# Optimization experiments

Hardware: AMD Instinct MI355X
Metric: run time of the kernel (lower is better)

Reference implementation:

```python
import jax, jax.numpy as jnp
import numpy as np

H, W = 576, 640            # image_height, image_width
V = 5                      # visible_patch_width (z-buffer visibility window)
P = 7                      # color_path_width (color splat window)
EPS = 1e-5                 # epsilon in splat weight denominator
BIG = 1e10                 # empty-pixel depth sentinel


def setup_inputs():
    key = jax.random.key(0)
    ks = jax.random.split(key, 6)
    B, N = 1, 200000
    x = jax.random.uniform(ks[0], (B, N), jnp.float32) * W
    y = jax.random.uniform(ks[1], (B, N), jnp.float32) * H
    z = jax.random.uniform(ks[2], (B, N), jnp.float32) * 9.0 + 1.0
    proj_points = jnp.stack([x, y, z], axis=-1)                 # [B,N,3]
    proj_color = jax.random.uniform(ks[3], (B, N, 3), jnp.float32)
    Imweights = jax.random.uniform(ks[4], (B, N, 1), jnp.float32)
    mask = jax.random.randint(ks[5], (B, N), 0, 2).astype(jnp.int32)
    threshold = jnp.array([0.05], dtype=jnp.float32)
    return {"proj_points": proj_points, "proj_color": proj_color,
            "Imweights": Imweights, "mask": mask, "threshold": threshold}


def _render(proj_points, proj_color, Imweights, mask, th):
    B, N, _ = proj_points.shape
    dt = proj_points.dtype
    x, y, z = proj_points[..., 0], proj_points[..., 1], proj_points[..., 2]
    px = jnp.floor(x).astype(jnp.int32)          # [B,N]
    py = jnp.floor(y).astype(jnp.int32)
    valid = (px >= 0) & (px < W) & (py >= 0) & (py < H) & (mask > 0)

    # ---- z-buffer: per-pixel min depth (scatter-min) ----
    flat = jnp.clip(py, 0, H - 1) * W + jnp.clip(px, 0, W - 1)   # [B,N]
    bidx = jnp.arange(B)[:, None]
    zput = jnp.where(valid, z, BIG)
    depth = jnp.full((B, H * W), BIG, dt).at[bidx, flat].min(zput).reshape(B, H, W)

    # min depth within VxV visibility patch around each pixel
    patch_min = jax.lax.reduce_window(depth, jnp.asarray(BIG, dt), jax.lax.min,
                                      (1, V, V), (1, 1, 1), "SAME")
    pm = patch_min[bidx, jnp.clip(py, 0, H - 1), jnp.clip(px, 0, W - 1)]  # [B,N]
    is_visible = jax.lax.stop_gradient(valid & (z <= pm + th))

    # ---- PxP color splat with inverse-square-distance weights ----
    r = P // 2
    offs = jnp.arange(-r, r + 1)
    oy, ox = [o.ravel() for o in jnp.meshgrid(offs, offs, indexing="ij")]  # [K]
    sx = px[..., None] + ox                                     # [B,N,K]
    sy = py[..., None] + oy
    inb = (sx >= 0) & (sx < W) & (sy >= 0) & (sy < H) & is_visible[..., None]
    dx = sx.astype(dt) + 0.5 - x[..., None]
    dy = sy.astype(dt) + 0.5 - y[..., None]
    w = jnp.where(inb, 1.0 / (dx * dx + dy * dy + EPS), 0.0)    # [B,N,K]
    sflat = jnp.clip(sy, 0, H - 1) * W + jnp.clip(sx, 0, W - 1)
    b3 = jnp.arange(B)[:, None, None]

    weight_image = jnp.zeros((B, H * W), dt).at[b3, sflat].add(w).reshape(B, H, W)
    color_image = (jnp.zeros((B, H * W, proj_color.shape[-1]), dt)
                   .at[b3, sflat].add(w[..., None] * proj_color[:, :, None, :])
                   .reshape(B, H, W, proj_color.shape[-1]))
    Imweights_image = (jnp.zeros((B, H * W, Imweights.shape[-1]), dt)
                       .at[b3, sflat].add(w[..., None] * Imweights[:, :, None, :])
                       .reshape(B, H, W, Imweights.shape[-1]))
    depth_image = jnp.where(depth >= BIG, jnp.zeros((), dt), depth)
    return depth_image, color_image, Imweights_image, weight_image, is_visible


def reference(proj_points, proj_color, Imweights, mask, threshold):
    th = jnp.reshape(threshold, ())
    return _render(proj_points, proj_color, Imweights, mask, th)
```

## Files before the change

### kernel.cpp

```cpp
#include <hip/hip_runtime.h>
#include <math.h>

#define IMG_H 576
#define IMG_W 640
#define IMG_HW (IMG_H * IMG_W)
#define BIGF 1e10f
#define EPSF 1e-5f

#define TS 16
#define TX (IMG_W / TS)
#define TY (IMG_H / TS)
#define NT (TX * TY)
#define CAP 512

#define PBX 32
#define PBY 8
#define LW (PBX + 4)
#define LH (PBY + 4)


__global__ void init_kernel(unsigned int* depth_bits, unsigned int* counters) {
    int i = blockIdx.x * blockDim.x + threadIdx.x;
    if (i < IMG_HW) depth_bits[i] = __float_as_uint(BIGF);
    if (i < NT) counters[i] = 0u;
}

__global__ void zbuf_kernel(const float* __restrict__ pts, const int* __restrict__ mask,
                            unsigned int* depth_bits, int N) {
    int n = blockIdx.x * blockDim.x + threadIdx.x;
    if (n >= N) return;
    float x = pts[3 * n + 0];
    float y = pts[3 * n + 1];
    float z = pts[3 * n + 2];
    int px = (int)floorf(x);
    int py = (int)floorf(y);
    if (px >= 0 && px < IMG_W && py >= 0 && py < IMG_H && mask[n] > 0)
        atomicMin(&depth_bits[py * IMG_W + px], __float_as_uint(z));
}

__global__ void __launch_bounds__(256)
patchmin_kernel(const unsigned int* __restrict__ depth_bits,
                float* __restrict__ patch_min,
                float* __restrict__ depth_image) {
    __shared__ float lds[LH * LW];
    int bx = (blockIdx.x % (IMG_W / PBX)) * PBX;
    int by = (blockIdx.x / (IMG_W / PBX)) * PBY;
    int tid = threadIdx.x;
    for (int i = tid; i < LH * LW; i += 256) {
        int gx = bx - 2 + (i % LW);
        int gy = by - 2 + (i / LW);
        float v = BIGF;
        if (gx >= 0 && gx < IMG_W && gy >= 0 && gy < IMG_H)
            v = __uint_as_float(depth_bits[gy * IMG_W + gx]);
        lds[i] = v;
    }
    __syncthreads();
    int lx = tid & (PBX - 1);
    int ly = tid >> 5;
    float m = BIGF;
    #pragma unroll
    for (int dy = 0; dy < 5; ++dy) {
        const float* row = lds + (ly + dy) * LW + lx;
        #pragma unroll
        for (int dx = 0; dx < 5; ++dx) m = fminf(m, row[dx]);
    }
    int p = (by + ly) * IMG_W + bx + lx;
    patch_min[p] = m;
    float d0 = lds[(ly + 2) * LW + lx + 2];
    depth_image[p] = (d0 >= BIGF) ? 0.0f : d0;
}

__global__ void vis_fill_kernel(const float* __restrict__ pts, const int* __restrict__ mask,
                                const float* __restrict__ thr,
                                const float* __restrict__ patch_min,
                                unsigned int* __restrict__ counters,
                                unsigned int* __restrict__ entries,
                                float* __restrict__ out_vis, int N) {
    int n = blockIdx.x * blockDim.x + threadIdx.x;
    if (n >= N) return;
    float x = pts[3 * n + 0];
    float y = pts[3 * n + 1];
    float z = pts[3 * n + 2];
    int px = (int)floorf(x);
    int py = (int)floorf(y);
    bool valid = (px >= 0) && (px < IMG_W) && (py >= 0) && (py < IMG_H) && (mask[n] > 0);
    bool vis = false;
    if (valid) {
        float pm = patch_min[py * IMG_W + px];
        vis = (z <= pm + thr[0]);
    }
    out_vis[n] = vis ? 1.0f : 0.0f;
    if (!vis) return;
    int xs0 = max(px - 3, 0), xs1 = min(px + 3, IMG_W - 1);
    int ys0 = max(py - 3, 0), ys1 = min(py + 3, IMG_H - 1);
    int tx0 = xs0 >> 4, tx1 = xs1 >> 4;
    int ty0 = ys0 >> 4, ty1 = ys1 >> 4;
    for (int ty = ty0; ty <= ty1; ++ty)
        for (int tx = tx0; tx <= tx1; ++tx) {
            int t = ty * TX + tx;
            unsigned int idx = atomicAdd(&counters[t], 1u);
            if (idx < CAP) entries[t * CAP + idx] = (unsigned int)n;
        }
}

__global__ void __launch_bounds__(256)
tile_splat_kernel(const float* __restrict__ pts, const float* __restrict__ color,
                  const float* __restrict__ imw,
                  const unsigned int* __restrict__ counters,
                  const unsigned int* __restrict__ entries,
                  float* __restrict__ out) {
    __shared__ float accW[TS * TS];
    __shared__ float accI[TS * TS];
    __shared__ float accR[TS * TS];
    __shared__ float accG[TS * TS];
    __shared__ float accB[TS * TS];
    int tid = threadIdx.x;
    if (tid < TS * TS) {
        accW[tid] = 0.0f; accI[tid] = 0.0f;
        accR[tid] = 0.0f; accG[tid] = 0.0f; accB[tid] = 0.0f;
    }
    __syncthreads();

    int tile = blockIdx.x;
    int tx0p = (tile % TX) * TS;
    int ty0p = (tile / TX) * TS;
    unsigned int count = min(counters[tile], (unsigned int)CAP);
    const unsigned int* list = entries + tile * CAP;

    for (unsigned int e = tid; e < count; e += blockDim.x) {
        int n = (int)list[e];
        float x = pts[3 * n + 0];
        float y = pts[3 * n + 1];
        int px = (int)floorf(x);
        int py = (int)floorf(y);
        float cr = color[3 * n + 0];
        float cg = color[3 * n + 1];
        float cb = color[3 * n + 2];
        float wv = imw[n];
        int sy0 = max(py - 3, ty0p), sy1 = min(py + 3, ty0p + TS - 1);
        int sx0 = max(px - 3, tx0p), sx1 = min(px + 3, tx0p + TS - 1);
        for (int sy = sy0; sy <= sy1; ++sy) {
            float dy = (float)sy + 0.5f - y;
            int ly = sy - ty0p;
            for (int sx = sx0; sx <= sx1; ++sx) {
                float dx = (float)sx + 0.5f - x;
                float w = 1.0f / (dx * dx + dy * dy + EPSF);
                int l = ly * TS + (sx - tx0p);
                atomicAdd(&accW[l], w);
                atomicAdd(&accI[l], w * wv);
                atomicAdd(&accR[l], w * cr);
                atomicAdd(&accG[l], w * cg);
                atomicAdd(&accB[l], w * cb);
            }
        }
    }
    __syncthreads();

    float* colimg = out + IMG_HW;
    float* imwimg = out + 4 * IMG_HW;
    float* wimg   = out + 5 * IMG_HW;
    if (tid < TS * TS) {
        int ly = tid / TS, lx = tid % TS;
        int p = (ty0p + ly) * IMG_W + tx0p + lx;
        wimg[p]   = accW[tid];
        imwimg[p] = accI[tid];
        colimg[3 * p + 0] = accR[tid];
        colimg[3 * p + 1] = accG[tid];
        colimg[3 * p + 2] = accB[tid];
    }
}

extern "C" void kernel_launch(void* const* d_in, const int* in_sizes, int n_in,
                              void* d_out, int out_size, void* d_ws, size_t ws_size,
                              hipStream_t stream) {
    const float* pts   = (const float*)d_in[0];
    const float* color = (const float*)d_in[1];
    const float* imw   = (const float*)d_in[2];
    const int*   mask  = (const int*)d_in[3];
    const float* thr   = (const float*)d_in[4];

    int N = in_sizes[3];

    unsigned int* ws_u = (unsigned int*)d_ws;
    unsigned int* depth_bits = ws_u;
    float*        patch_min  = (float*)(ws_u + IMG_HW);
    unsigned int* counters   = ws_u + 2 * IMG_HW;
    unsigned int* entries    = counters + NT;

    float* out = (float*)d_out;
    float* out_vis = out + 6 * IMG_HW;

    const int B = 256;
    init_kernel<<<(IMG_HW + B - 1) / B, B, 0, stream>>>(depth_bits, counters);
    zbuf_kernel<<<(N + B - 1) / B, B, 0, stream>>>(pts, mask, depth_bits, N);
    patchmin_kernel<<<(IMG_W / PBX) * (IMG_H / PBY), 256, 0, stream>>>(depth_bits, patch_min, out);
    vis_fill_kernel<<<(N + B - 1) / B, B, 0, stream>>>(pts, mask, thr, patch_min,
                                                       counters, entries, out_vis, N);
    tile_splat_kernel<<<NT, 256, 0, stream>>>(pts, color, imw, counters, entries, out);
}
```

Measured before the change: 111.6 us.

## Switch tile splat from point-parallel LDS atomics to pixel-parallel gather

The splat kernel now assigns one thread per tile pixel instead of one thread per point. Each chunk of up to 256 point attributes is staged in shared memory, and every thread loops over all staged points, accumulating weights in registers when the point lies within the 7x7 window. This removes five shared-memory float atomics per contribution, at the cost of each thread testing every point in the tile list. The depth-image write moves from the patch-min kernel into the splat kernel. Summation order per pixel becomes deterministic.

Result: faster. 94.04 us (-15.7%).

```diff
diff --git a/kernel.cpp b/kernel.cpp
--- a/kernel.cpp
+++ b/kernel.cpp
@@ -40,8 +40,7 @@
 
 __global__ void __launch_bounds__(256)
 patchmin_kernel(const unsigned int* __restrict__ depth_bits,
-                float* __restrict__ patch_min,
-                float* __restrict__ depth_image) {
+                float* __restrict__ patch_min) {
     __shared__ float lds[LH * LW];
     int bx = (blockIdx.x % (IMG_W / PBX)) * PBX;
     int by = (blockIdx.x / (IMG_W / PBX)) * PBY;
@@ -64,10 +63,7 @@
         #pragma unroll
         for (int dx = 0; dx < 5; ++dx) m = fminf(m, row[dx]);
     }
-    int p = (by + ly) * IMG_W + bx + lx;
-    patch_min[p] = m;
-    float d0 = lds[(ly + 2) * LW + lx + 2];
-    depth_image[p] = (d0 >= BIGF) ? 0.0f : d0;
+    patch_min[(by + ly) * IMG_W + bx + lx] = m;
 }
 
 __global__ void vis_fill_kernel(const float* __restrict__ pts, const int* __restrict__ mask,
@@ -108,66 +104,65 @@
                   const float* __restrict__ imw,
                   const unsigned int* __restrict__ counters,
                   const unsigned int* __restrict__ entries,
+                  const unsigned int* __restrict__ depth_bits,
                   float* __restrict__ out) {
-    __shared__ float accW[TS * TS];
-    __shared__ float accI[TS * TS];
-    __shared__ float accR[TS * TS];
-    __shared__ float accG[TS * TS];
-    __shared__ float accB[TS * TS];
-    int tid = threadIdx.x;
-    if (tid < TS * TS) {
-        accW[tid] = 0.0f; accI[tid] = 0.0f;
-        accR[tid] = 0.0f; accG[tid] = 0.0f; accB[tid] = 0.0f;
-    }
-    __syncthreads();
-
+    __shared__ float sx_[256], sy_[256], sr_[256], sg_[256], sb_[256], si_[256];
     int tile = blockIdx.x;
     int tx0p = (tile % TX) * TS;
     int ty0p = (tile / TX) * TS;
+    int tid = threadIdx.x;
+    int lx = tid & (TS - 1);
+    int ly = tid >> 4;
+    int gx = tx0p + lx;
+    int gy = ty0p + ly;
+    float pxf = (float)gx + 0.5f;
+    float pyf = (float)gy + 0.5f;
+
+    float aW = 0.0f, aI = 0.0f, aR = 0.0f, aG = 0.0f, aB = 0.0f;
+
     unsigned int count = min(counters[tile], (unsigned int)CAP);
     const unsigned int* list = entries + tile * CAP;
 
-    for (unsigned int e = tid; e < count; e += blockDim.x) {
-        int n = (int)list[e];
-        float x = pts[3 * n + 0];
-        float y = pts[3 * n + 1];
-        int px = (int)floorf(x);
-        int py = (int)floorf(y);
-        float cr = color[3 * n + 0];
-        float cg = color[3 * n + 1];
-        float cb = color[3 * n + 2];
-        float wv = imw[n];
-        int sy0 = max(py - 3, ty0p), sy1 = min(py + 3, ty0p + TS - 1);
-        int sx0 = max(px - 3, tx0p), sx1 = min(px + 3, tx0p + TS - 1);
-        for (int sy = sy0; sy <= sy1; ++sy) {
-            float dy = (float)sy + 0.5f - y;
-            int ly = sy - ty0p;
-            for (int sx = sx0; sx <= sx1; ++sx) {
-                float dx = (float)sx + 0.5f - x;
+    for (unsigned int base = 0; base < count; base += 256u) {
+        unsigned int chunk = min(256u, count - base);
+        __syncthreads();
+        if (tid < chunk) {
+            int n = (int)list[base + tid];
+            sx_[tid] = pts[3 * n + 0];
+            sy_[tid] = pts[3 * n + 1];
+            sr_[tid] = color[3 * n + 0];
+            sg_[tid] = color[3 * n + 1];
+            sb_[tid] = color[3 * n + 2];
+            si_[tid] = imw[n];
+        }
+        __syncthreads();
+        for (unsigned int e = 0; e < chunk; ++e) {
+            float x = sx_[e];
+            float y = sy_[e];
+            int px = (int)floorf(x);
+            int py = (int)floorf(y);
+            if ((unsigned int)(gx - px + 3) <= 6u && (unsigned int)(gy - py + 3) <= 6u) {
+                float dx = pxf - x;
+                float dy = pyf - y;
                 float w = 1.0f / (dx * dx + dy * dy + EPSF);
-                int l = ly * TS + (sx - tx0p);
-                atomicAdd(&accW[l], w);
-                atomicAdd(&accI[l], w * wv);
-                atomicAdd(&accR[l], w * cr);
-                atomicAdd(&accG[l], w * cg);
-                atomicAdd(&accB[l], w * cb);
+                aW += w;
+                aI += w * si_[e];
+                aR += w * sr_[e];
+                aG += w * sg_[e];
+                aB += w * sb_[e];
             }
         }
     }
-    __syncthreads();
 
+    int p = gy * IMG_W + gx;
+    float d0 = __uint_as_float(depth_bits[p]);
+    out[p] = (d0 >= BIGF) ? 0.0f : d0;
     float* colimg = out + IMG_HW;
-    float* imwimg = out + 4 * IMG_HW;
-    float* wimg   = out + 5 * IMG_HW;
-    if (tid < TS * TS) {
-        int ly = tid / TS, lx = tid % TS;
-        int p = (ty0p + ly) * IMG_W + tx0p + lx;
-        wimg[p]   = accW[tid];
-        imwimg[p] = accI[tid];
-        colimg[3 * p + 0] = accR[tid];
-        colimg[3 * p + 1] = accG[tid];
-        colimg[3 * p + 2] = accB[tid];
-    }
+    colimg[3 * p + 0] = aR;
+    colimg[3 * p + 1] = aG;
+    colimg[3 * p + 2] = aB;
+    out[4 * IMG_HW + p] = aI;
+    out[5 * IMG_HW + p] = aW;
 }
 
 extern "C" void kernel_launch(void* const* d_in, const int* in_sizes, int n_in,
@@ -193,8 +188,9 @@
     const int B = 256;
     init_kernel<<<(IMG_HW + B - 1) / B, B, 0, stream>>>(depth_bits, counters);
     zbuf_kernel<<<(N + B - 1) / B, B, 0, stream>>>(pts, mask, depth_bits, N);
-    patchmin_kernel<<<(IMG_W / PBX) * (IMG_H / PBY), 256, 0, stream>>>(depth_bits, patch_min, out);
+    patchmin_kernel<<<(IMG_W / PBX) * (IMG_H / PBY), 256, 0, stream>>>(depth_bits, patch_min);
     vis_fill_kernel<<<(N + B - 1) / B, B, 0, stream>>>(pts, mask, thr, patch_min,
                                                        counters, entries, out_vis, N);
-    tile_splat_kernel<<<NT, 256, 0, stream>>>(pts, color, imw, counters, entries, out);
+    tile_splat_kernel<<<NT, 256, 0, stream>>>(pts, color, imw, counters, entries,
+                                              depth_bits, out);
 }
```
